# Optimization experiments

Measured on AMD Instinct MI355X. Metric: run time of the kernel, lower is better.

## Reference

```python
import jax, jax.numpy as jnp
import numpy as np

SCORER_BIAS = 0.0
LN_EPS = 1e-5


def setup_inputs() -> dict:
    key = jax.random.key(0)
    k0, k1, k2 = jax.random.split(key, 3)
    B, L, D, H = 8, 8192, 1024, 256
    features = jax.random.normal(k0, (B, L, D), dtype=jnp.float32)
    gamma = jnp.ones((D,), jnp.float32)
    beta = jnp.zeros((D,), jnp.float32)
    W1 = (jax.random.normal(k1, (D, H)) * (1.0 / np.sqrt(D))).astype(jnp.float32)
    b1 = jnp.zeros((H,), jnp.float32)
    W2 = (jax.random.normal(k2, (H, 1)) * (1.0 / np.sqrt(H))).astype(jnp.float32)
    b2 = jnp.zeros((1,), jnp.float32)
    return {"features": features, "gamma": gamma, "beta": beta,
            "W1": W1, "b1": b1, "W2": W2, "b2": b2, "k": 512}


def reference(features, gamma, beta, W1, b1, W2, b2, k):
    # LayerNorm over last dim D
    mu = jnp.mean(features, axis=-1, keepdims=True)
    var = jnp.mean(jnp.square(features - mu), axis=-1, keepdims=True)
    x = (features - mu) * jax.lax.rsqrt(var + LN_EPS) * gamma + beta  # [B,L,D]
    # small MLP scorer: Linear -> GELU(exact, matches torch default) -> Linear
    h = jax.nn.gelu(jnp.einsum('bld,dh->blh', x, W1) + b1, approximate=False)
    scores = (jnp.einsum('blh,ho->blo', h, W2) + b2)[..., 0] + SCORER_BIAS  # [B,L]
    # per-row top-k (torch.topk semantics: largest, sorted)
    _, idx = jax.lax.top_k(scores, k)  # [B,k] int32
    # batched gather of original (un-normalized) features
    selected = jnp.take_along_axis(features, idx[..., None], axis=1)  # [B,k,D]
    return selected, scores, idx
```

## Files before the change

kernel.cpp:

```cpp
#include <hip/hip_runtime.h>
#include <math.h>

#define Dk 1024
#define Hk 256
#define Lk 8192
#define Bk 8
#define MTOT (Bk*Lk)

typedef _Float16 f16;
typedef __attribute__((ext_vector_type(8))) _Float16 f16x8;
typedef __attribute__((ext_vector_type(4))) float f32x4;
typedef unsigned long long u64;

#define AKG 520
#define ASP (8*AKG)
#define ABUF (2*ASP)

__global__ __launch_bounds__(1024) void prep_split(
    const float* __restrict__ W1, const float* __restrict__ gamma,
    const float* __restrict__ beta, f16* __restrict__ W1F,
    float* __restrict__ Spart, float* __restrict__ Tpart) {
  __shared__ float ps[1024], pt[1024];
  const int b = blockIdx.x, t = threadIdx.x;
  float sa = 0.f, ta = 0.f;
  #pragma unroll
  for (int j = 0; j < 4; ++j) {
    int idx = j * 65536 + b * 1024 + t;
    int d = idx >> 8, h = idx & 255;
    float w = W1[idx];
    float g = gamma[d];
    sa = fmaf(g, w, sa);
    ta = fmaf(beta[d], w, ta);
    float wg = g * w;
    f16 whi = (f16)wg;
    f16 wlp = (f16)((wg - (float)whi) * 2048.f);
    int ks = d >> 6, kg = (d >> 3) & 7, kk = d & 7;
    int nf = h >> 4, nn = h & 15;
    size_t base = ((((size_t)ks * 2) * 16 + nf) * 8 + kg) * 128 + nn * 8 + kk;
    W1F[base] = whi;
    W1F[base + 16384] = wlp;
  }
  ps[t] = sa; pt[t] = ta;
  __syncthreads();
  if (t < 256) {
    Spart[b * 256 + t] = ps[t] + ps[t + 256] + ps[t + 512] + ps[t + 768];
    Tpart[b * 256 + t] = pt[t] + pt[t + 256] + pt[t + 512] + pt[t + 768];
  }
}

__global__ __launch_bounds__(256) void prep_combine(
    const float* __restrict__ Spart, const float* __restrict__ Tpart,
    const float* __restrict__ b1, float* __restrict__ S, float* __restrict__ Tb) {
  int j = threadIdx.x;
  float s = 0.f, t = 0.f;
  for (int b = 0; b < 64; ++b) { s += Spart[b * 256 + j]; t += Tpart[b * 256 + j]; }
  S[j] = s;
  Tb[j] = t + b1[j];
}

__global__ __launch_bounds__(512, 2) void scores_mfma(
    const float* __restrict__ F, const f16* __restrict__ W1F,
    const float* __restrict__ S, const float* __restrict__ Tb,
    const float* __restrict__ W2, const float* __restrict__ b2,
    float* __restrict__ scores_out) {
  __shared__ f16 As[2][ABUF];
  __shared__ float smu[64], srs[64];
  __shared__ float sred[64][4];

  const int tid = threadIdx.x;
  const int RM = blockIdx.x * 64;
  const int wid = tid >> 6, lane = tid & 63;
  const int wm = wid & 1, wn = wid >> 1;
  const int lg = lane >> 4, l15 = lane & 15;

  const int arow = tid >> 3, kg = tid & 7;
  const float* Aptr = F + (size_t)(RM + arow) * Dk + kg * 8;

  const int aoff0 = lg * AKG + (wm * 32 + l15) * 8;
  const int bwoff = (wn * 4) * 1024 + lg * 128 + l15 * 8;

  f32x4 accA[2][4], accB[2][4];
  #pragma unroll
  for (int i = 0; i < 2; ++i)
    #pragma unroll
    for (int j = 0; j < 4; ++j) {
      accA[i][j] = (f32x4){0.f, 0.f, 0.f, 0.f};
      accB[i][j] = (f32x4){0.f, 0.f, 0.f, 0.f};
    }

  float rsum = 0.f, rsq = 0.f;

#define SPLIT_STORE(buf, av0, av1)                                             \
  {                                                                            \
    float xx[8] = {av0.x, av0.y, av0.z, av0.w, av1.x, av1.y, av1.z, av1.w};    \
    f16x8 vhi, vlo;                                                            \
    _Pragma("unroll")                                                          \
    for (int e = 0; e < 8; ++e) {                                              \
      float x = xx[e];                                                         \
      rsum += x; rsq = fmaf(x, x, rsq);                                        \
      f16 hi = (f16)x;                                                         \
      vhi[e] = hi;                                                             \
      vlo[e] = (f16)((x - (float)hi) * 2048.f);                                \
    }                                                                          \
    *reinterpret_cast<f16x8*>(&As[buf][kg * AKG + arow * 8]) = vhi;            \
    *reinterpret_cast<f16x8*>(&As[buf][ASP + kg * AKG + arow * 8]) = vlo;      \
  }

  float4 av0 = *reinterpret_cast<const float4*>(Aptr);
  float4 av1 = *reinterpret_cast<const float4*>(Aptr + 4);
  SPLIT_STORE(0, av0, av1)
  av0 = *reinterpret_cast<const float4*>(Aptr + 64);
  av1 = *reinterpret_cast<const float4*>(Aptr + 68);
  __syncthreads();

  for (int s = 0; s < 16; ++s) {
    const int cur = s & 1;
    const f16* bstep = W1F + (size_t)s * 32768 + bwoff;
    f16x8 whi[4], wlp[4];
    #pragma unroll
    for (int nf = 0; nf < 4; ++nf) {
      whi[nf] = *reinterpret_cast<const f16x8*>(bstep + nf * 1024);
      wlp[nf] = *reinterpret_cast<const f16x8*>(bstep + nf * 1024 + 16384);
    }
    if (s < 15) {
      SPLIT_STORE(cur ^ 1, av0, av1)
      if (s < 14) {
        av0 = *reinterpret_cast<const float4*>(Aptr + (s + 2) * 64);
        av1 = *reinterpret_cast<const float4*>(Aptr + (s + 2) * 64 + 4);
      }
    }
    {
      const f16* ab = &As[cur][aoff0];
      f16x8 ahi0 = *reinterpret_cast<const f16x8*>(ab);
      f16x8 ahi1 = *reinterpret_cast<const f16x8*>(ab + 128);
      f16x8 axl0 = *reinterpret_cast<const f16x8*>(ab + ASP);
      f16x8 axl1 = *reinterpret_cast<const f16x8*>(ab + ASP + 128);
      #pragma unroll
      for (int nf = 0; nf < 4; ++nf) {
        f16x8 wlr = wlp[nf] * (f16)0.00048828125f;
        accA[0][nf] = __builtin_amdgcn_mfma_f32_16x16x32_f16(ahi0, whi[nf], accA[0][nf], 0, 0, 0);
        accB[0][nf] = __builtin_amdgcn_mfma_f32_16x16x32_f16(ahi0, wlp[nf], accB[0][nf], 0, 0, 0);
        accB[0][nf] = __builtin_amdgcn_mfma_f32_16x16x32_f16(axl0, whi[nf], accB[0][nf], 0, 0, 0);
        accB[0][nf] = __builtin_amdgcn_mfma_f32_16x16x32_f16(axl0, wlr, accB[0][nf], 0, 0, 0);
        accA[1][nf] = __builtin_amdgcn_mfma_f32_16x16x32_f16(ahi1, whi[nf], accA[1][nf], 0, 0, 0);
        accB[1][nf] = __builtin_amdgcn_mfma_f32_16x16x32_f16(ahi1, wlp[nf], accB[1][nf], 0, 0, 0);
        accB[1][nf] = __builtin_amdgcn_mfma_f32_16x16x32_f16(axl1, whi[nf], accB[1][nf], 0, 0, 0);
        accB[1][nf] = __builtin_amdgcn_mfma_f32_16x16x32_f16(axl1, wlr, accB[1][nf], 0, 0, 0);
      }
    }
    #pragma unroll
    for (int nf = 0; nf < 4; ++nf) {
      whi[nf] = *reinterpret_cast<const f16x8*>(bstep + nf * 1024 + 512);
      wlp[nf] = *reinterpret_cast<const f16x8*>(bstep + nf * 1024 + 512 + 16384);
    }
    {
      const f16* ab = &As[cur][aoff0 + 4 * AKG];
      f16x8 ahi0 = *reinterpret_cast<const f16x8*>(ab);
      f16x8 ahi1 = *reinterpret_cast<const f16x8*>(ab + 128);
      f16x8 axl0 = *reinterpret_cast<const f16x8*>(ab + ASP);
      f16x8 axl1 = *reinterpret_cast<const f16x8*>(ab + ASP + 128);
      #pragma unroll
      for (int nf = 0; nf < 4; ++nf) {
        f16x8 wlr = wlp[nf] * (f16)0.00048828125f;
        accA[0][nf] = __builtin_amdgcn_mfma_f32_16x16x32_f16(ahi0, whi[nf], accA[0][nf], 0, 0, 0);
        accB[0][nf] = __builtin_amdgcn_mfma_f32_16x16x32_f16(ahi0, wlp[nf], accB[0][nf], 0, 0, 0);
        accB[0][nf] = __builtin_amdgcn_mfma_f32_16x16x32_f16(axl0, whi[nf], accB[0][nf], 0, 0, 0);
        accB[0][nf] = __builtin_amdgcn_mfma_f32_16x16x32_f16(axl0, wlr, accB[0][nf], 0, 0, 0);
        accA[1][nf] = __builtin_amdgcn_mfma_f32_16x16x32_f16(ahi1, whi[nf], accA[1][nf], 0, 0, 0);
        accB[1][nf] = __builtin_amdgcn_mfma_f32_16x16x32_f16(ahi1, wlp[nf], accB[1][nf], 0, 0, 0);
        accB[1][nf] = __builtin_amdgcn_mfma_f32_16x16x32_f16(axl1, whi[nf], accB[1][nf], 0, 0, 0);
        accB[1][nf] = __builtin_amdgcn_mfma_f32_16x16x32_f16(axl1, wlr, accB[1][nf], 0, 0, 0);
      }
    }
    __syncthreads();
  }

  rsum += __shfl_xor(rsum, 1); rsum += __shfl_xor(rsum, 2); rsum += __shfl_xor(rsum, 4);
  rsq  += __shfl_xor(rsq, 1);  rsq  += __shfl_xor(rsq, 2);  rsq  += __shfl_xor(rsq, 4);
  if ((tid & 7) == 0) {
    float mu  = rsum * (1.f / 1024.f);
    float var = rsq * (1.f / 1024.f) - mu * mu;
    smu[arow] = mu;
    srs[arow] = rsqrtf(var + 1e-5f);
  }
  __syncthreads();

  float s2[4], tb2[4], w2v[4];
  #pragma unroll
  for (int nf = 0; nf < 4; ++nf) {
    int col = (wn * 4 + nf) * 16 + l15;
    s2[nf] = S[col]; tb2[nf] = Tb[col]; w2v[nf] = W2[col];
  }
  #pragma unroll
  for (int mf = 0; mf < 2; ++mf) {
    const int rbase = wm * 32 + mf * 16 + lg * 4;
    #pragma unroll
    for (int reg = 0; reg < 4; ++reg) {
      const int row = rbase + reg;
      float mu = smu[row], rs = srs[row];
      float part = 0.f;
      #pragma unroll
      for (int nf = 0; nf < 4; ++nf) {
        float val = accA[mf][nf][reg] + accB[mf][nf][reg] * (1.f / 2048.f);
        float hpre = rs * val - rs * mu * s2[nf] + tb2[nf];
        float g = 0.5f * hpre * (1.f + erff(hpre * 0.70710678118654752f));
        part = fmaf(g, w2v[nf], part);
      }
      part += __shfl_xor(part, 1); part += __shfl_xor(part, 2);
      part += __shfl_xor(part, 4); part += __shfl_xor(part, 8);
      if (l15 == 0) sred[row][wn] = part;
    }
  }
  __syncthreads();
  if (tid < 64) {
    float sc = b2[0] + sred[tid][0] + sred[tid][1] + sred[tid][2] + sred[tid][3];
    scores_out[RM + tid] = sc;
  }
}

__global__ __launch_bounds__(512) void topk_stage1(
    const float* __restrict__ scores, u64* __restrict__ kout) {
  __shared__ u64 keys[1024];
  const int blk = blockIdx.x;
  const int batch = blk >> 3, chunk = blk & 7;
  const int t = threadIdx.x;
  #pragma unroll
  for (int j = 0; j < 2; ++j) {
    int i = t + j * 512;
    int gi = chunk * 1024 + i;
    unsigned u = __float_as_uint(scores[(size_t)batch * Lk + gi]);
    unsigned mono = (u & 0x80000000u) ? ~u : (u | 0x80000000u);
    keys[i] = ((u64)(~mono) << 32) | (unsigned)gi;
  }
  __syncthreads();
  for (int size = 2; size <= 1024; size <<= 1) {
    for (int stride = size >> 1; stride > 0; stride >>= 1) {
      int lo = ((t & ~(stride - 1)) << 1) | (t & (stride - 1));
      int hi = lo + stride;
      bool up = ((lo & size) == 0);
      u64 a = keys[lo], c = keys[hi];
      if ((a > c) == up) { keys[lo] = c; keys[hi] = a; }
      __syncthreads();
    }
  }
  kout[(size_t)blk * 512 + t] = keys[t];
}

__global__ __launch_bounds__(512) void topk_stage2(
    const u64* __restrict__ kin, int k,
    float* __restrict__ idx_f, int* __restrict__ idx_i) {
  __shared__ u64 kk[4096];
  __shared__ u64 tmp[2048];
  const int b = blockIdx.x, t = threadIdx.x;
  #pragma unroll
  for (int j = 0; j < 8; ++j) kk[t + j * 512] = kin[(size_t)b * 4096 + t + j * 512];
  __syncthreads();
  #pragma unroll
  for (int j = 0; j < 4; ++j) {
    u64 a = kk[j * 1024 + t];
    u64 c = kk[j * 1024 + 512 + (511 - t)];
    tmp[j * 512 + t] = a < c ? a : c;
  }
  __syncthreads();
  for (int stride = 256; stride > 0; stride >>= 1) {
    #pragma unroll
    for (int w = 0; w < 2; ++w) {
      int p = t + w * 512;
      int r = p >> 8, q = p & 255;
      int lo = r * 512 + (((q & ~(stride - 1)) << 1) | (q & (stride - 1)));
      u64 a = tmp[lo], c = tmp[lo + stride];
      if (a > c) { tmp[lo] = c; tmp[lo + stride] = a; }
    }
    __syncthreads();
  }
  if (t < 512) {
    int j = t >> 8 >> 1;
  }
  #pragma unroll
  for (int j = 0; j < 2; ++j) {
    u64 a = tmp[j * 1024 + t];
    u64 c = tmp[j * 1024 + 512 + (511 - t)];
    kk[j * 512 + t] = a < c ? a : c;
  }
  __syncthreads();
  for (int stride = 256; stride > 0; stride >>= 1) {
    int r = t >> 8, q = t & 255;
    int lo = r * 512 + (((q & ~(stride - 1)) << 1) | (q & (stride - 1)));
    u64 a = kk[lo], c = kk[lo + stride];
    if (a > c) { kk[lo] = c; kk[lo + stride] = a; }
    __syncthreads();
  }
  {
    u64 a = kk[t];
    u64 c = kk[512 + (511 - t)];
    tmp[t] = a < c ? a : c;
  }
  __syncthreads();
  for (int stride = 256; stride > 0; stride >>= 1) {
    if (t < 256) {
      int lo = ((t & ~(stride - 1)) << 1) | (t & (stride - 1));
      u64 a = tmp[lo], c = tmp[lo + stride];
      if (a > c) { tmp[lo] = c; tmp[lo + stride] = a; }
    }
    __syncthreads();
  }
  if (t < k) {
    int id = (int)(tmp[t] & 0xFFFFFFFFu);
    idx_f[(size_t)b * k + t] = (float)id;
    idx_i[(size_t)b * k + t] = id;
  }
}

__global__ __launch_bounds__(256) void gather_kernel(
    const float* __restrict__ F, const int* __restrict__ idx,
    float* __restrict__ out, int k) {
  int row = blockIdx.x;
  int b = row / k;
  int id = idx[row];
  const float4* src = reinterpret_cast<const float4*>(F + ((size_t)b * Lk + id) * Dk);
  float4* dst = reinterpret_cast<float4*>(out + (size_t)row * Dk);
  dst[threadIdx.x] = src[threadIdx.x];
}

extern "C" void kernel_launch(void* const* d_in, const int* in_sizes, int n_in,
                              void* d_out, int out_size, void* d_ws, size_t ws_size,
                              hipStream_t stream) {
  const float* F     = (const float*)d_in[0];
  const float* gamma = (const float*)d_in[1];
  const float* beta  = (const float*)d_in[2];
  const float* W1    = (const float*)d_in[3];
  const float* b1    = (const float*)d_in[4];
  const float* W2    = (const float*)d_in[5];
  const float* b2    = (const float*)d_in[6];
  int k = (out_size - Bk * Lk) / (Bk * Dk + Bk);

  float* out_sel = (float*)d_out;
  float* out_sc  = out_sel + (size_t)Bk * k * Dk;
  float* out_idx = out_sc + (size_t)Bk * Lk;

  f16*   W1F   = (f16*)d_ws;
  u64*   kout  = (u64*)((char*)d_ws + (1 << 20));
  float* Spart = (float*)((char*)kout + 262144);
  float* Tpart = Spart + 16384;
  float* Sp    = Tpart + 16384;
  float* Tbp   = Sp + Hk;
  int*   idxi  = (int*)(Tbp + Hk);

  hipLaunchKernelGGL(prep_split,   dim3(64),        dim3(1024), 0, stream,
                     W1, gamma, beta, W1F, Spart, Tpart);
  hipLaunchKernelGGL(prep_combine, dim3(1),         dim3(Hk),   0, stream,
                     Spart, Tpart, b1, Sp, Tbp);
  hipLaunchKernelGGL(scores_mfma,  dim3(MTOT / 64), dim3(512),  0, stream,
                     F, W1F, Sp, Tbp, W2, b2, out_sc);
  hipLaunchKernelGGL(topk_stage1,  dim3(64),        dim3(512),  0, stream,
                     out_sc, kout);
  hipLaunchKernelGGL(topk_stage2,  dim3(Bk),        dim3(512),  0, stream,
                     kout, k, out_idx, idxi);
  hipLaunchKernelGGL(gather_kernel, dim3(Bk * k),   dim3(256),  0, stream,
                     F, idxi, out_sel, k);
}
```

Baseline: 187.6 us.

## Drop lo*lo MFMA term and cut register pressure for four blocks per CU

Removes the fourth MFMA (x_lo times scaled w_lo) from the split-fp16 product, so each tile now issues three MFMAs instead of four. Weight fragments are loaded two at a time instead of four, and the split-store no longer builds a local array. This lowers VGPR use so the launch bound can request four blocks per CU instead of two, aiming for more latency hiding and less matrix work. The risk is a small accuracy loss from the dropped correction term, which could flip near-tied top-k indices, and possible spills if the compiler cannot fit the tighter register budget.

```diff
diff --git a/kernel.cpp b/kernel.cpp
--- a/kernel.cpp
+++ b/kernel.cpp
@@ -58,7 +58,12 @@
   Tb[j] = t + b1[j];
 }
 
-__global__ __launch_bounds__(512, 2) void scores_mfma(
+#define MM3(aA, aB, ah, ax, wh, wl)                                            \
+  aA = __builtin_amdgcn_mfma_f32_16x16x32_f16(ah, wh, aA, 0, 0, 0);            \
+  aB = __builtin_amdgcn_mfma_f32_16x16x32_f16(ah, wl, aB, 0, 0, 0);            \
+  aB = __builtin_amdgcn_mfma_f32_16x16x32_f16(ax, wh, aB, 0, 0, 0);
+
+__global__ __launch_bounds__(512, 4) void scores_mfma(
     const float* __restrict__ F, const f16* __restrict__ W1F,
     const float* __restrict__ S, const float* __restrict__ Tb,
     const float* __restrict__ W2, const float* __restrict__ b2,
@@ -92,11 +97,13 @@
 
 #define SPLIT_STORE(buf, av0, av1)                                             \
   {                                                                            \
-    float xx[8] = {av0.x, av0.y, av0.z, av0.w, av1.x, av1.y, av1.z, av1.w};    \
     f16x8 vhi, vlo;                                                            \
     _Pragma("unroll")                                                          \
     for (int e = 0; e < 8; ++e) {                                              \
-      float x = xx[e];                                                         \
+      float x = (e < 4) ? ((e == 0) ? av0.x : (e == 1) ? av0.y                 \
+                           : (e == 2) ? av0.z : av0.w)                         \
+                        : ((e == 4) ? av1.x : (e == 5) ? av1.y                 \
+                           : (e == 6) ? av1.z : av1.w);                        \
       rsum += x; rsq = fmaf(x, x, rsq);                                        \
       f16 hi = (f16)x;                                                         \
       vhi[e] = hi;                                                             \
@@ -115,62 +122,60 @@
 
   for (int s = 0; s < 16; ++s) {
     const int cur = s & 1;
-    const f16* bstep = W1F + (size_t)s * 32768 + bwoff;
-    f16x8 whi[4], wlp[4];
-    #pragma unroll
-    for (int nf = 0; nf < 4; ++nf) {
-      whi[nf] = *reinterpret_cast<const f16x8*>(bstep + nf * 1024);
-      wlp[nf] = *reinterpret_cast<const f16x8*>(bstep + nf * 1024 + 16384);
-    }
-    if (s < 15) {
-      SPLIT_STORE(cur ^ 1, av0, av1)
-      if (s < 14) {
-        av0 = *reinterpret_cast<const float4*>(Aptr + (s + 2) * 64);
-        av1 = *reinterpret_cast<const float4*>(Aptr + (s + 2) * 64 + 4);
-      }
-    }
+    const f16* bs = W1F + (size_t)s * 32768 + bwoff;
+
     {
+      f16x8 wh0 = *reinterpret_cast<const f16x8*>(bs);
+      f16x8 wh1 = *reinterpret_cast<const f16x8*>(bs + 1024);
+      f16x8 wl0 = *reinterpret_cast<const f16x8*>(bs + 16384);
+      f16x8 wl1 = *reinterpret_cast<const f16x8*>(bs + 17408);
       const f16* ab = &As[cur][aoff0];
       f16x8 ahi0 = *reinterpret_cast<const f16x8*>(ab);
       f16x8 ahi1 = *reinterpret_cast<const f16x8*>(ab + 128);
       f16x8 axl0 = *reinterpret_cast<const f16x8*>(ab + ASP);
       f16x8 axl1 = *reinterpret_cast<const f16x8*>(ab + ASP + 128);
-      #pragma unroll
-      for (int nf = 0; nf < 4; ++nf) {
-        f16x8 wlr = wlp[nf] * (f16)0.00048828125f;
-        accA[0][nf] = __builtin_amdgcn_mfma_f32_16x16x32_f16(ahi0, whi[nf], accA[0][nf], 0, 0, 0);
-        accB[0][nf] = __builtin_amdgcn_mfma_f32_16x16x32_f16(ahi0, wlp[nf], accB[0][nf], 0, 0, 0);
-        accB[0][nf] = __builtin_amdgcn_mfma_f32_16x16x32_f16(axl0, whi[nf], accB[0][nf], 0, 0, 0);
-        accB[0][nf] = __builtin_amdgcn_mfma_f32_16x16x32_f16(axl0, wlr, accB[0][nf], 0, 0, 0);
-        accA[1][nf] = __builtin_amdgcn_mfma_f32_16x16x32_f16(ahi1, whi[nf], accA[1][nf], 0, 0, 0);
-        accB[1][nf] = __builtin_amdgcn_mfma_f32_16x16x32_f16(ahi1, wlp[nf], accB[1][nf], 0, 0, 0);
-        accB[1][nf] = __builtin_amdgcn_mfma_f32_16x16x32_f16(axl1, whi[nf], accB[1][nf], 0, 0, 0);
-        accB[1][nf] = __builtin_amdgcn_mfma_f32_16x16x32_f16(axl1, wlr, accB[1][nf], 0, 0, 0);
+      if (s < 15) {
+        SPLIT_STORE(cur ^ 1, av0, av1)
+        if (s < 14) {
+          av0 = *reinterpret_cast<const float4*>(Aptr + (s + 2) * 64);
+          av1 = *reinterpret_cast<const float4*>(Aptr + (s + 2) * 64 + 4);
+        }
       }
-    }
-    #pragma unroll
-    for (int nf = 0; nf < 4; ++nf) {
-      whi[nf] = *reinterpret_cast<const f16x8*>(bstep + nf * 1024 + 512);
-      wlp[nf] = *reinterpret_cast<const f16x8*>(bstep + nf * 1024 + 512 + 16384);
+      MM3(accA[0][0], accB[0][0], ahi0, axl0, wh0, wl0)
+      MM3(accA[1][0], accB[1][0], ahi1, axl1, wh0, wl0)
+      MM3(accA[0][1], accB[0][1], ahi0, axl0, wh1, wl1)
+      MM3(accA[1][1], accB[1][1], ahi1, axl1, wh1, wl1)
+      wh0 = *reinterpret_cast<const f16x8*>(bs + 2048);
+      wh1 = *reinterpret_cast<const f16x8*>(bs + 3072);
+      wl0 = *reinterpret_cast<const f16x8*>(bs + 2048 + 16384);
+      wl1 = *reinterpret_cast<const f16x8*>(bs + 3072 + 16384);
+      MM3(accA[0][2], accB[0][2], ahi0, axl0, wh0, wl0)
+      MM3(accA[1][2], accB[1][2], ahi1, axl1, wh0, wl0)
+      MM3(accA[0][3], accB[0][3], ahi0, axl0, wh1, wl1)
+      MM3(accA[1][3], accB[1][3], ahi1, axl1, wh1, wl1)
     }
     {
+      f16x8 wh0 = *reinterpret_cast<const f16x8*>(bs + 512);
+      f16x8 wh1 = *reinterpret_cast<const f16x8*>(bs + 512 + 1024);
+      f16x8 wl0 = *reinterpret_cast<const f16x8*>(bs + 512 + 16384);
+      f16x8 wl1 = *reinterpret_cast<const f16x8*>(bs + 512 + 17408);
       const f16* ab = &As[cur][aoff0 + 4 * AKG];
       f16x8 ahi0 = *reinterpret_cast<const f16x8*>(ab);
       f16x8 ahi1 = *reinterpret_cast<const f16x8*>(ab + 128);
       f16x8 axl0 = *reinterpret_cast<const f16x8*>(ab + ASP);
       f16x8 axl1 = *reinterpret_cast<const f16x8*>(ab + ASP + 128);
-      #pragma unroll
-      for (int nf = 0; nf < 4; ++nf) {
-        f16x8 wlr = wlp[nf] * (f16)0.00048828125f;
-        accA[0][nf] = __builtin_amdgcn_mfma_f32_16x16x32_f16(ahi0, whi[nf], accA[0][nf], 0, 0, 0);
-        accB[0][nf] = __builtin_amdgcn_mfma_f32_16x16x32_f16(ahi0, wlp[nf], accB[0][nf], 0, 0, 0);
-        accB[0][nf] = __builtin_amdgcn_mfma_f32_16x16x32_f16(axl0, whi[nf], accB[0][nf], 0, 0, 0);
-        accB[0][nf] = __builtin_amdgcn_mfma_f32_16x16x32_f16(axl0, wlr, accB[0][nf], 0, 0, 0);
-        accA[1][nf] = __builtin_amdgcn_mfma_f32_16x16x32_f16(ahi1, whi[nf], accA[1][nf], 0, 0, 0);
-        accB[1][nf] = __builtin_amdgcn_mfma_f32_16x16x32_f16(ahi1, wlp[nf], accB[1][nf], 0, 0, 0);
-        accB[1][nf] = __builtin_amdgcn_mfma_f32_16x16x32_f16(axl1, whi[nf], accB[1][nf], 0, 0, 0);
-        accB[1][nf] = __builtin_amdgcn_mfma_f32_16x16x32_f16(axl1, wlr, accB[1][nf], 0, 0, 0);
-      }
+      MM3(accA[0][0], accB[0][0], ahi0, axl0, wh0, wl0)
+      MM3(accA[1][0], accB[1][0], ahi1, axl1, wh0, wl0)
+      MM3(accA[0][1], accB[0][1], ahi0, axl0, wh1, wl1)
+      MM3(accA[1][1], accB[1][1], ahi1, axl1, wh1, wl1)
+      wh0 = *reinterpret_cast<const f16x8*>(bs + 512 + 2048);
+      wh1 = *reinterpret_cast<const f16x8*>(bs + 512 + 3072);
+      wl0 = *reinterpret_cast<const f16x8*>(bs + 512 + 2048 + 16384);
+      wl1 = *reinterpret_cast<const f16x8*>(bs + 512 + 3072 + 16384);
+      MM3(accA[0][2], accB[0][2], ahi0, axl0, wh0, wl0)
+      MM3(accA[1][2], accB[1][2], ahi1, axl1, wh0, wl0)
+      MM3(accA[0][3], accB[0][3], ahi0, axl0, wh1, wl1)
+      MM3(accA[1][3], accB[1][3], ahi1, axl1, wh1, wl1)
     }
     __syncthreads();
   }
@@ -273,9 +278,6 @@
     }
     __syncthreads();
   }
-  if (t < 512) {
-    int j = t >> 8 >> 1;
-  }
   #pragma unroll
   for (int j = 0; j < 2; ++j) {
     u64 a = tmp[j * 1024 + t];
```

Result: faster. 161.8 us (-13.7%).
